# Performance work log

Hardware: AMD Instinct MI355X
Metric: run time of the kernel (lower is better)

The kernel has to match this reference:

```python
import jax, jax.numpy as jnp
import numpy as np
from jax import lax

EPS = 1e-07
B, H, W = 32, 120, 120
N_PRIM, PRIM_DIM = 16, 8          # 16 capsule types, 8-d pose
N_SEC, SEC_DIM = 10, 16           # 10 secondary capsules, 16-d
FLAT = 9216                       # 16 * 24 * 24
R_ITERS = 3
REC_DIM = H * W * 3               # 43200


def _conv(x, w, b, stride):
    # NHWC input, HWIO kernel, VALID padding
    y = lax.conv_general_dilated(x, w, (stride, stride), 'VALID',
                                 dimension_numbers=('NHWC', 'HWIO', 'NHWC'))
    return y + b


def _squash(s):
    s_norm = jnp.linalg.norm(s, axis=-1, keepdims=True)
    sq = jnp.square(s_norm)
    return sq / (1.0 + sq) * s / (s_norm + EPS)


def setup_inputs() -> dict:
    key = jax.random.key(0)
    ks = jax.random.split(key, 13)
    p = lambda k, shp, s=0.05: (jax.random.normal(k, shp, dtype=jnp.float32) * s)
    inp = {
        'input_x': jax.random.normal(ks[0], (B, H, W, 3), dtype=jnp.float32),
        'y':       jax.random.uniform(ks[1], (B, N_SEC), dtype=jnp.float32),
        'conv1_w': p(ks[2], (9, 9, 3, 256)),
        'conv1_b': jnp.zeros((256,), jnp.float32),
        'conv2_w': p(ks[3], (9, 9, 256, N_PRIM * PRIM_DIM)),
        'conv2_b': jnp.zeros((N_PRIM * PRIM_DIM,), jnp.float32),
        'w_pose':  p(ks[4], (1, FLAT, N_SEC, SEC_DIM, PRIM_DIM)),
        'w1': p(ks[5], (N_SEC * SEC_DIM, 512)), 'b1': jnp.zeros((512,), jnp.float32),
        'w2': p(ks[6], (512, 1024)),            'b2': jnp.zeros((1024,), jnp.float32),
        'w3': p(ks[7], (1024, REC_DIM)),        'b3': jnp.zeros((REC_DIM,), jnp.float32),
    }
    return inp


def reference(input_x, y, conv1_w, conv1_b, conv2_w, conv2_b, w_pose,
              w1, b1, w2, b2, w3, b3):
    b = input_x.shape[0]
    # feature extraction
    x = jax.nn.relu(_conv(input_x, conv1_w, conv1_b, 2))   # [B,56,56,256]
    x = _conv(x, conv2_w, conv2_b, 2)                      # [B,24,24,128]
    u = x.reshape(b, FLAT, PRIM_DIM)                       # [B,9216,8]
    # u_hat[b,n,c,d] = sum_p w_pose[0,n,c,d,p] * u[b,n,p]
    u_hat = jnp.einsum('ncdp,bnp->bncd', w_pose[0], u)     # [B,9216,10,16]
    # dynamic routing
    logits = jnp.zeros((b, FLAT, N_SEC, 1), jnp.float32)
    v = None
    for _ in range(R_ITERS):
        c = jax.nn.softmax(logits, axis=-2)                # over secondary caps
        s = jnp.sum(c * u_hat, axis=1, keepdims=True)      # [B,1,10,16]
        v = _squash(s)
        agreement = jnp.sum(u_hat * v, axis=-1, keepdims=True)  # [B,9216,10,1]
        logits = logits + agreement
    # masking + reconstruction
    mask = y[:, None, :, None]                             # [B,1,10,1]
    v_flat = (mask * v).reshape(b, -1)                     # [B,160]
    h = jax.nn.relu(v_flat @ w1 + b1)
    h = jax.nn.relu(h @ w2 + b2)
    rec = jax.nn.sigmoid(h @ w3 + b3)                      # [B,43200]
    return v, rec
```

## Files before the change

kernel.cpp:

```cpp
#include <hip/hip_runtime.h>
#include <hip/hip_bf16.h>

typedef unsigned short u16;
typedef unsigned int   u32;
typedef __attribute__((ext_vector_type(8))) __bf16 bf16x8;
typedef __attribute__((ext_vector_type(4))) float  f32x4;

#define EPSQ 1e-7f
#define KSPLIT 9
#define KPB 2304
#define KSTEPS 72
#define FC3SPL 8

#define GLDS16(gp, lp) __builtin_amdgcn_global_load_lds( \
    (const __attribute__((address_space(1))) void*)(gp), \
    (__attribute__((address_space(3))) void*)(lp), 16, 0, 0)

__device__ __forceinline__ u16 f2bf(float f){
  u32 u = __float_as_uint(f);
  u32 r = (u + 0x7fffu + ((u >> 16) & 1u)) >> 16;
  return (u16)r;
}
__device__ __forceinline__ float bf2f(u16 h){ return __uint_as_float(((u32)h) << 16); }
__device__ __forceinline__ float blo(u32 w){ return __uint_as_float(w << 16); }
__device__ __forceinline__ float bhi(u32 w){ return __uint_as_float(w & 0xffff0000u); }

__global__ __launch_bounds__(256) void k_im2col(const float* __restrict__ x, u16* __restrict__ A1){
  const int id = blockIdx.x*256 + threadIdx.x;
  const int m  = id >> 5;
  const int s  = id & 31;
  const int b  = m / 3136;
  const int r  = m - b*3136;
  const int oy = r / 56;
  const int ox = r - oy*56;
  const float* xb = x + ((size_t)b*120 + 2*oy)*120*3 + 2*ox*3;
  u16 vals[8];
  #pragma unroll
  for (int j=0;j<8;++j){
    int k = s*8 + j;
    if (k < 243){
      int ky = k / 27;
      int rem = k - ky*27;
      vals[j] = f2bf(xb[(size_t)ky*360 + rem]);
    } else vals[j] = 0;
  }
  *reinterpret_cast<uint4*>(A1 + (size_t)m*256 + s*8) = *reinterpret_cast<uint4*>(vals);
}

__global__ __launch_bounds__(256) void k_wt1(const float* __restrict__ w, u16* __restrict__ wt){
  __shared__ float tile[32][33];
  const int k0 = blockIdx.x*32;
  const int c0 = blockIdx.y*32;
  const int c  = threadIdx.x & 31;
  const int r8 = threadIdx.x >> 5;
  #pragma unroll
  for (int rr=0; rr<4; ++rr){
    int r = r8*4+rr;
    tile[r][c] = (k0+r < 243) ? w[(size_t)(k0+r)*256 + c0 + c] : 0.f;
  }
  __syncthreads();
  #pragma unroll
  for (int rr=0; rr<4; ++rr){
    int r = r8*4+rr;
    wt[(size_t)(c0+r)*256 + k0 + c] = f2bf(tile[c][r]);
  }
}

__global__ __launch_bounds__(256) void k_gemm1(const u16* __restrict__ A1,
    const u16* __restrict__ w1t, const float* __restrict__ bias, u16* __restrict__ a1b){
  __shared__ __align__(16) u16 As[2][4096];
  __shared__ __align__(16) u16 Bs[2][4096];
  const int t  = threadIdx.x;
  const int bx = blockIdx.x;
  const int by = blockIdx.y;
  const int row0 = t>>2, slot = t&3;
  const int wid = t>>6, lane = t&63;
  const int wr = wid>>1, wc = wid&1, lr = lane&15, lq = lane>>4;
  const size_t srcA0 = (size_t)(bx*128 + row0)*256 + slot*8;
  const size_t srcA1 = srcA0 + (size_t)64*256;
  const size_t srcB0 = (size_t)(by*128 + row0)*256 + slot*8;
  const size_t srcB1 = srcB0 + (size_t)64*256;
  f32x4 acc[4][4];
  #pragma unroll
  for (int i=0;i<4;++i)
    #pragma unroll
    for (int j=0;j<4;++j) acc[i][j] = (f32x4){0.f,0.f,0.f,0.f};

  auto stage = [&](int step, int buf){
    const int k0 = step*32;
    GLDS16(A1 + srcA0 + k0, &As[buf][wid*512]);
    GLDS16(A1 + srcA1 + k0, &As[buf][wid*512 + 2048]);
    GLDS16(w1t + srcB0 + k0, &Bs[buf][wid*512]);
    GLDS16(w1t + srcB1 + k0, &Bs[buf][wid*512 + 2048]);
  };
  auto compute = [&](int buf){
    bf16x8 af[4], bfv[4];
    #pragma unroll
    for (int mi=0;mi<4;++mi)
      af[mi] = *reinterpret_cast<const bf16x8*>(&As[buf][(wr*64 + mi*16 + lr)*32 + lq*8]);
    #pragma unroll
    for (int ni=0;ni<4;++ni)
      bfv[ni] = *reinterpret_cast<const bf16x8*>(&Bs[buf][(wc*64 + ni*16 + lr)*32 + lq*8]);
    #pragma unroll
    for (int mi=0;mi<4;++mi)
      #pragma unroll
      for (int ni=0;ni<4;++ni)
        acc[mi][ni] = __builtin_amdgcn_mfma_f32_16x16x32_bf16(af[mi], bfv[ni], acc[mi][ni], 0, 0, 0);
  };

  stage(0, 0);
  __syncthreads();
  for (int step=0; step<8; step+=2){
    stage(step+1, 1);
    compute(0);
    __syncthreads();
    if (step+2 < 8) stage(step+2, 0);
    compute(1);
    __syncthreads();
  }

  #pragma unroll
  for (int ni=0;ni<4;++ni){
    int colg = by*128 + wc*64 + ni*16 + lr;
    float bv = bias[colg];
    #pragma unroll
    for (int mi=0;mi<4;++mi){
      #pragma unroll
      for (int r=0;r<4;++r){
        int rowg = bx*128 + wr*64 + mi*16 + lq*4 + r;
        float v = fmaxf(acc[mi][ni][r] + bv, 0.f);
        a1b[(size_t)rowg*256 + colg] = f2bf(v);
      }
    }
  }
}

__global__ __launch_bounds__(256) void k_wt(const float* __restrict__ w, u16* __restrict__ wt){
  __shared__ float tile[32][33];
  const int k0 = blockIdx.x*32;
  const int c0 = blockIdx.y*32;
  const int c  = threadIdx.x & 31;
  const int r8 = threadIdx.x >> 5;
  #pragma unroll
  for (int rr=0; rr<4; ++rr){
    int r = r8*4+rr;
    tile[r][c] = w[(size_t)(k0+r)*128 + c0 + c];
  }
  __syncthreads();
  #pragma unroll
  for (int rr=0; rr<4; ++rr){
    int r = r8*4+rr;
    wt[(size_t)(c0+r)*20736 + k0 + c] = f2bf(tile[c][r]);
  }
}

__global__ __launch_bounds__(256) void k_conv2(const u16* __restrict__ a1b,
    const u16* __restrict__ w2t, float* __restrict__ part){
  __shared__ __align__(16) u16 As[2][4096];
  __shared__ __align__(16) u16 Bs[2][4096];
  const int t  = threadIdx.x;
  const int bx = blockIdx.x;
  const int ks = blockIdx.y;
  const int row0 = t>>2, slot = t&3;
  int gA[2]; int gB[2];
  #pragma unroll
  for (int q=0;q<2;++q){
    int m  = bx*128 + row0 + q*64;
    int bb = m/576; int r = m - bb*576; int oy = r/24; int ox = r - oy*24;
    gA[q] = ((bb*56 + 2*oy)*56 + 2*ox)*256 + slot*8;
    int col = row0 + q*64;
    gB[q] = col*20736 + slot*8;
  }
  const int wid = t>>6, lane = t&63;
  const int wr = wid>>1, wc = wid&1, lr = lane&15, lq = lane>>4;
  f32x4 acc[4][4];
  #pragma unroll
  for (int i=0;i<4;++i)
    #pragma unroll
    for (int j=0;j<4;++j) acc[i][j] = (f32x4){0.f,0.f,0.f,0.f};
  const int kbase = ks*KPB;

  auto stage = [&](int step, int buf){
    const int k0  = kbase + step*32;
    const int kk  = k0 >> 8;
    const int ky  = kk/9;
    const int kx  = kk - ky*9;
    const int ic0 = k0 & 255;
    const int soff = (ky*56 + kx)*256 + ic0;
    GLDS16(a1b + gA[0] + soff, &As[buf][wid*512]);
    GLDS16(a1b + gA[1] + soff, &As[buf][wid*512 + 2048]);
    GLDS16(w2t + gB[0] + k0,  &Bs[buf][wid*512]);
    GLDS16(w2t + gB[1] + k0,  &Bs[buf][wid*512 + 2048]);
  };
  auto compute = [&](int buf){
    bf16x8 af[4], bfv[4];
    #pragma unroll
    for (int mi=0;mi<4;++mi)
      af[mi] = *reinterpret_cast<const bf16x8*>(&As[buf][(wr*64 + mi*16 + lr)*32 + lq*8]);
    #pragma unroll
    for (int ni=0;ni<4;++ni)
      bfv[ni] = *reinterpret_cast<const bf16x8*>(&Bs[buf][(wc*64 + ni*16 + lr)*32 + lq*8]);
    #pragma unroll
    for (int mi=0;mi<4;++mi)
      #pragma unroll
      for (int ni=0;ni<4;++ni)
        acc[mi][ni] = __builtin_amdgcn_mfma_f32_16x16x32_bf16(af[mi], bfv[ni], acc[mi][ni], 0, 0, 0);
  };

  stage(0, 0);
  __syncthreads();
  for (int step=0; step<KSTEPS; step+=2){
    stage(step+1, 1);
    compute(0);
    __syncthreads();
    if (step+2 < KSTEPS) stage(step+2, 0);
    compute(1);
    __syncthreads();
  }

  const size_t base = ((size_t)ks*18432 + (size_t)bx*128)*128;
  #pragma unroll
  for (int mi=0;mi<4;++mi){
    #pragma unroll
    for (int ni=0;ni<4;++ni){
      int col = wc*64 + ni*16 + lr;
      #pragma unroll
      for (int r=0;r<4;++r){
        int row = wr*64 + mi*16 + lq*4 + r;
        part[base + (size_t)row*128 + col] = acc[mi][ni][r];
      }
    }
  }
}

__global__ __launch_bounds__(256) void k_comb(const float* __restrict__ part,
    const float* __restrict__ bias, float* __restrict__ u){
  const int i4 = blockIdx.x*256 + threadIdx.x;
  const float4* b4 = reinterpret_cast<const float4*>(bias);
  float4 s = b4[i4 & 31];
  const float4* p4 = reinterpret_cast<const float4*>(part);
  #pragma unroll
  for (int ks=0; ks<KSPLIT; ++ks){
    float4 p = p4[(size_t)ks*589824 + i4];
    s.x += p.x; s.y += p.y; s.z += p.z; s.w += p.w;
  }
  reinterpret_cast<float4*>(u)[i4] = s;
}

__global__ __launch_bounds__(256) void k_uhat(const float* __restrict__ u,
    const float* __restrict__ wpose, u16* __restrict__ uhat){
  __shared__ float Wn[1280];
  __shared__ float us[256];
  const int n = blockIdx.x;
  const int t = threadIdx.x;
  #pragma unroll
  for (int j=0;j<5;++j) Wn[t + j*256] = wpose[(size_t)n*1280 + t + j*256];
  us[t] = u[((size_t)(t>>3)*9216 + n)*8 + (t&7)];
  __syncthreads();
  const int b = t>>3, d0 = (t&7)*2;
  float uv[8];
  #pragma unroll
  for (int p=0;p<8;++p) uv[p] = us[b*8+p];
  for (int c=0;c<10;++c){
    const float* w0 = &Wn[(c*16 + d0)*8];
    float v0=0.f, v1=0.f;
    #pragma unroll
    for (int p=0;p<8;++p){ v0 = fmaf(w0[p], uv[p], v0); v1 = fmaf(w0[8+p], uv[p], v1); }
    u32 pk = (u32)f2bf(v0) | ((u32)f2bf(v1) << 16);
    *reinterpret_cast<u32*>(uhat + ((((size_t)b*10 + c)*9216 + n)*16 + d0)) = pk;
  }
}

template<int ITER>
__global__ __launch_bounds__(256) void k_route(const u16* __restrict__ uhat,
    const float* __restrict__ spin, float* __restrict__ logi,
    float* __restrict__ spout){
  const int ch = blockIdx.x;
  const int b  = blockIdx.y;
  const int t  = threadIdx.x;
  const int n  = ch*256 + t;
  __shared__ float vl[160];
  __shared__ float sq[160];
  __shared__ float wlds[10][257];
  __shared__ float pacc[10][16][33];
  if (ITER >= 2){
    float sv = 0.f;
    if (t < 160){
      #pragma unroll 4
      for (int c2=0;c2<36;++c2) sv += spin[((size_t)c2*32 + b)*160 + t];
      sq[t] = sv*sv;
    }
    __syncthreads();
    if (t < 160){
      int cc = t >> 4;
      float ss = 0.f;
      #pragma unroll
      for (int j=0;j<16;++j) ss += sq[cc*16 + j];
      float nrm = sqrtf(ss);
      vl[t] = (ss/(1.f+ss)) * sv / (nrm + EPSQ);
    }
    __syncthreads();
  }
  float w[10];
  if (ITER == 1){
    #pragma unroll
    for (int c=0;c<10;++c) w[c] = 0.1f;
  } else {
    float l[10];
    #pragma unroll
    for (int c=0;c<10;++c){
      const u16* up = uhat + ((((size_t)b*10 + c)*9216 + n) << 4);
      const uint4 q0 = *reinterpret_cast<const uint4*>(up);
      const uint4 q1 = *reinterpret_cast<const uint4*>(up + 8);
      const float* v = &vl[c*16];
      float dot = blo(q0.x)*v[0] + bhi(q0.x)*v[1]
                + blo(q0.y)*v[2] + bhi(q0.y)*v[3]
                + blo(q0.z)*v[4] + bhi(q0.z)*v[5]
                + blo(q0.w)*v[6] + bhi(q0.w)*v[7]
                + blo(q1.x)*v[8] + bhi(q1.x)*v[9]
                + blo(q1.y)*v[10]+ bhi(q1.y)*v[11]
                + blo(q1.z)*v[12]+ bhi(q1.z)*v[13]
                + blo(q1.w)*v[14]+ bhi(q1.w)*v[15];
      size_t li = ((size_t)b*10 + c)*9216 + n;
      float lc = dot;
      if (ITER == 3) lc += logi[li];
      if (ITER == 2) logi[li] = lc;
      l[c] = lc;
    }
    float mx = l[0];
    #pragma unroll
    for (int c=1;c<10;++c) mx = fmaxf(mx, l[c]);
    float s = 0.f;
    #pragma unroll
    for (int c=0;c<10;++c){ w[c] = __expf(l[c]-mx); s += w[c]; }
    float inv = 1.f/s;
    #pragma unroll
    for (int c=0;c<10;++c) w[c] *= inv;
  }
  #pragma unroll
  for (int c=0;c<10;++c) wlds[c][t] = w[c];
  __syncthreads();

  const int nl = t>>3, dp = t&7;
  float a0[10], a1[10];
  #pragma unroll
  for (int c=0;c<10;++c){ a0[c]=0.f; a1[c]=0.f; }
  #pragma unroll
  for (int c=0;c<10;++c){
    const u32* ub = reinterpret_cast<const u32*>(
        uhat + ((((size_t)b*10 + c)*9216 + (size_t)ch*256) << 4));
    float acc0 = 0.f, acc1 = 0.f;
    #pragma unroll
    for (int chunk=0; chunk<8; ++chunk){
      u32 v = ub[chunk*256 + t];
      float wv = wlds[c][chunk*32 + nl];
      acc0 = fmaf(wv, blo(v), acc0);
      acc1 = fmaf(wv, bhi(v), acc1);
    }
    a0[c] = acc0; a1[c] = acc1;
  }
  #pragma unroll
  for (int c=0;c<10;++c){
    pacc[c][2*dp  ][nl] = a0[c];
    pacc[c][2*dp+1][nl] = a1[c];
  }
  __syncthreads();
  if (t < 160){
    const int c = t >> 4, d = t & 15;
    float acc = 0.f;
    #pragma unroll
    for (int j=0;j<32;++j) acc += pacc[c][d][j];
    spout[((size_t)ch*32 + b)*160 + t] = acc;
  }
}

__global__ __launch_bounds__(1024) void k_head(const float* __restrict__ y,
    const float* __restrict__ spin, const float* __restrict__ w1,
    const float* __restrict__ b1, const float* __restrict__ w2,
    const float* __restrict__ b2, float* __restrict__ dout_v,
    float* __restrict__ h2T){
  const int b = blockIdx.x;
  const int t = threadIdx.x;
  __shared__ float vl[160];
  __shared__ float sq[160];
  __shared__ float h1s[512];
  float sv = 0.f;
  if (t < 160){
    #pragma unroll 4
    for (int c2=0;c2<36;++c2) sv += spin[((size_t)c2*32 + b)*160 + t];
    sq[t] = sv*sv;
  }
  __syncthreads();
  if (t < 160){
    int cc = t >> 4;
    float ss = 0.f;
    #pragma unroll
    for (int j=0;j<16;++j) ss += sq[cc*16 + j];
    float nrm = sqrtf(ss);
    float vv = (ss/(1.f+ss)) * sv / (nrm + EPSQ);
    dout_v[(size_t)b*160 + t] = vv;
    vl[t] = vv * y[b*10 + cc];
  }
  __syncthreads();
  if (t < 512){
    float acc = b1[t];
    for (int k=0;k<160;++k) acc = fmaf(vl[k], w1[(size_t)k*512 + t], acc);
    h1s[t] = fmaxf(acc, 0.f);
  }
  __syncthreads();
  float acc = b2[t];
  for (int k=0;k<512;++k) acc = fmaf(h1s[k], w2[(size_t)k*1024 + t], acc);
  h2T[(size_t)t*32 + b] = fmaxf(acc, 0.f);
}

__global__ __launch_bounds__(256) void k_fc3p(const float* __restrict__ h2T,
    const float* __restrict__ w3, float* __restrict__ fp){
  __shared__ float4 hs4[128][8];
  const int t  = threadIdx.x;
  const int oc = blockIdx.x*256 + t;
  const int ks = blockIdx.y;
  const float4* src = reinterpret_cast<const float4*>(h2T + (size_t)ks*128*32);
  #pragma unroll
  for (int r=0;r<4;++r)
    (&hs4[0][0])[t + r*256] = src[t + r*256];
  __syncthreads();
  const bool ok = oc < 43200;
  float a[32];
  #pragma unroll
  for (int b=0;b<32;++b) a[b] = 0.f;
  const size_t wbase = (size_t)ks*128*43200 + (size_t)(ok ? oc : 0);
  #pragma unroll 4
  for (int k=0;k<128;++k){
    float wv = w3[wbase + (size_t)k*43200];
    #pragma unroll
    for (int q=0;q<8;++q){
      float4 hv = hs4[k][q];
      a[q*4+0] = fmaf(hv.x, wv, a[q*4+0]);
      a[q*4+1] = fmaf(hv.y, wv, a[q*4+1]);
      a[q*4+2] = fmaf(hv.z, wv, a[q*4+2]);
      a[q*4+3] = fmaf(hv.w, wv, a[q*4+3]);
    }
  }
  if (ok){
    #pragma unroll
    for (int b=0;b<32;++b) fp[(size_t)(ks*32 + b)*43200 + oc] = a[b];
  }
}

__global__ __launch_bounds__(256) void k_fc3f(const float* __restrict__ fp,
    const float* __restrict__ b3, float* __restrict__ outr){
  const int i4 = blockIdx.x*256 + threadIdx.x;
  if (i4 >= 345600) return;
  const int b = i4 / 10800, oc4 = i4 - b*10800;
  const float4* b34 = reinterpret_cast<const float4*>(b3);
  float4 s = b34[oc4];
  const float4* fp4 = reinterpret_cast<const float4*>(fp);
  #pragma unroll
  for (int ks=0;ks<FC3SPL;++ks){
    float4 p = fp4[(size_t)(ks*32 + b)*10800 + oc4];
    s.x += p.x; s.y += p.y; s.z += p.z; s.w += p.w;
  }
  float4 o;
  o.x = 1.f/(1.f + __expf(-s.x));
  o.y = 1.f/(1.f + __expf(-s.y));
  o.z = 1.f/(1.f + __expf(-s.z));
  o.w = 1.f/(1.f + __expf(-s.w));
  reinterpret_cast<float4*>(outr)[i4] = o;
}

extern "C" void kernel_launch(void* const* d_in, const int* in_sizes, int n_in,
                              void* d_out, int out_size, void* d_ws, size_t ws_size,
                              hipStream_t stream){
  (void)in_sizes; (void)n_in; (void)out_size; (void)ws_size;
  const float* x     = (const float*)d_in[0];
  const float* y     = (const float*)d_in[1];
  const float* c1w   = (const float*)d_in[2];
  const float* c1b   = (const float*)d_in[3];
  const float* c2w   = (const float*)d_in[4];
  const float* c2b   = (const float*)d_in[5];
  const float* wpose = (const float*)d_in[6];
  const float* w1    = (const float*)d_in[7];
  const float* b1    = (const float*)d_in[8];
  const float* w2    = (const float*)d_in[9];
  const float* b2    = (const float*)d_in[10];
  const float* w3    = (const float*)d_in[11];
  const float* b3    = (const float*)d_in[12];
  float* out = (float*)d_out;

  char* ws = (char*)d_ws;
  u16*   a1bp  = (u16*)(ws + 0);
  u16*   A1col = (u16*)(ws + 52000000);
  float* partp = (float*)(ws + 52000000);
  u16*   uhatp = (u16*)(ws + 0);
  u16*   w1tp  = (u16*)(ws + 138000000);
  u16*   w2tp  = (u16*)(ws + 138500000);
  float* up    = (float*)(ws + 144000000);
  float* logip = (float*)(ws + 154000000);
  float* spA   = (float*)(ws + 166000000);
  float* spB   = (float*)(ws + 166800000);
  float* h2Tp  = (float*)(ws + 167600000);
  float* fc3pp = (float*)(ws + 0);

  k_im2col<<<dim3(12544),  256, 0, stream>>>(x, A1col);
  k_wt1   <<<dim3(8,8),    256, 0, stream>>>(c1w, w1tp);
  k_wt    <<<dim3(648,4),  256, 0, stream>>>(c2w, w2tp);
  k_gemm1 <<<dim3(784,2),  256, 0, stream>>>(A1col, w1tp, c1b, a1bp);
  k_conv2 <<<dim3(144,KSPLIT), 256, 0, stream>>>(a1bp, w2tp, partp);
  k_comb  <<<dim3(2304),   256, 0, stream>>>(partp, c2b, up);
  k_uhat  <<<dim3(9216),   256, 0, stream>>>(up, wpose, uhatp);

  k_route<1><<<dim3(36,32), 256, 0, stream>>>(uhatp, spB, logip, spA);
  k_route<2><<<dim3(36,32), 256, 0, stream>>>(uhatp, spA, logip, spB);
  k_route<3><<<dim3(36,32), 256, 0, stream>>>(uhatp, spB, logip, spA);

  k_head <<<dim3(32),   1024, 0, stream>>>(y, spA, w1, b1, w2, b2, out, h2Tp);
  k_fc3p <<<dim3(169,FC3SPL), 256, 0, stream>>>(h2Tp, w3, fc3pp);
  k_fc3f <<<dim3(1350), 256, 0, stream>>>(fc3pp, b3, out + 5120);
}
```

Baseline: 538.6 us.

## Use vmcnt-based double buffering in GEMMs and split head kernel across blocks

The conv1 and conv2 GEMM main loops now issue the next stage's global-to-LDS loads and then wait with s_waitcnt vmcnt(4) plus raw s_barrier, replacing full __syncthreads drains. The intent is to keep prefetches in flight while the current tile is computed. Separately, the head kernel moves from 32 blocks of 1024 threads to 32x4 blocks of 256 threads, so the FC2 output columns are spread over more workgroups. Each block recomputes FC1 redundantly, and the vmcnt(4) value depends on each thread issuing exactly four loads per stage.

```diff
diff --git a/kernel.cpp b/kernel.cpp
--- a/kernel.cpp
+++ b/kernel.cpp
@@ -109,14 +109,20 @@
   };
 
   stage(0, 0);
-  __syncthreads();
-  for (int step=0; step<8; step+=2){
-    stage(step+1, 1);
-    compute(0);
-    __syncthreads();
-    if (step+2 < 8) stage(step+2, 0);
-    compute(1);
-    __syncthreads();
+  int cur = 0;
+  for (int step=0; step<8; ++step){
+    if (step+1 < 8){
+      stage(step+1, cur^1);
+      asm volatile("s_waitcnt vmcnt(4)" ::: "memory");
+    } else {
+      asm volatile("s_waitcnt vmcnt(0)" ::: "memory");
+    }
+    __builtin_amdgcn_s_barrier();
+    __builtin_amdgcn_sched_barrier(0);
+    compute(cur);
+    __builtin_amdgcn_s_barrier();
+    __builtin_amdgcn_sched_barrier(0);
+    cur ^= 1;
   }
 
   #pragma unroll
@@ -208,14 +214,20 @@
   };
 
   stage(0, 0);
-  __syncthreads();
-  for (int step=0; step<KSTEPS; step+=2){
-    stage(step+1, 1);
-    compute(0);
-    __syncthreads();
-    if (step+2 < KSTEPS) stage(step+2, 0);
-    compute(1);
-    __syncthreads();
+  int cur = 0;
+  for (int step=0; step<KSTEPS; ++step){
+    if (step+1 < KSTEPS){
+      stage(step+1, cur^1);
+      asm volatile("s_waitcnt vmcnt(4)" ::: "memory");
+    } else {
+      asm volatile("s_waitcnt vmcnt(0)" ::: "memory");
+    }
+    __builtin_amdgcn_s_barrier();
+    __builtin_amdgcn_sched_barrier(0);
+    compute(cur);
+    __builtin_amdgcn_s_barrier();
+    __builtin_amdgcn_sched_barrier(0);
+    cur ^= 1;
   }
 
   const size_t base = ((size_t)ks*18432 + (size_t)bx*128)*128;
@@ -374,12 +386,13 @@
   }
 }
 
-__global__ __launch_bounds__(1024) void k_head(const float* __restrict__ y,
+__global__ __launch_bounds__(256) void k_head(const float* __restrict__ y,
     const float* __restrict__ spin, const float* __restrict__ w1,
     const float* __restrict__ b1, const float* __restrict__ w2,
     const float* __restrict__ b2, float* __restrict__ dout_v,
     float* __restrict__ h2T){
   const int b = blockIdx.x;
+  const int q = blockIdx.y;
   const int t = threadIdx.x;
   __shared__ float vl[160];
   __shared__ float sq[160];
@@ -398,19 +411,22 @@
     for (int j=0;j<16;++j) ss += sq[cc*16 + j];
     float nrm = sqrtf(ss);
     float vv = (ss/(1.f+ss)) * sv / (nrm + EPSQ);
-    dout_v[(size_t)b*160 + t] = vv;
+    if (q == 0) dout_v[(size_t)b*160 + t] = vv;
     vl[t] = vv * y[b*10 + cc];
   }
   __syncthreads();
-  if (t < 512){
-    float acc = b1[t];
-    for (int k=0;k<160;++k) acc = fmaf(vl[k], w1[(size_t)k*512 + t], acc);
-    h1s[t] = fmaxf(acc, 0.f);
-  }
-  __syncthreads();
-  float acc = b2[t];
-  for (int k=0;k<512;++k) acc = fmaf(h1s[k], w2[(size_t)k*1024 + t], acc);
-  h2T[(size_t)t*32 + b] = fmaxf(acc, 0.f);
+  #pragma unroll
+  for (int j=0;j<2;++j){
+    const int oc = j*256 + t;
+    float acc = b1[oc];
+    for (int k=0;k<160;++k) acc = fmaf(vl[k], w1[(size_t)k*512 + oc], acc);
+    h1s[oc] = fmaxf(acc, 0.f);
+  }
+  __syncthreads();
+  const int oc2 = q*256 + t;
+  float acc = b2[oc2];
+  for (int k=0;k<512;++k) acc = fmaf(h1s[k], w2[(size_t)k*1024 + oc2], acc);
+  h2T[(size_t)oc2*32 + b] = fmaxf(acc, 0.f);
 }
 
 __global__ __launch_bounds__(256) void k_fc3p(const float* __restrict__ h2T,
@@ -513,7 +529,7 @@
   k_route<2><<<dim3(36,32), 256, 0, stream>>>(uhatp, spA, logip, spB);
   k_route<3><<<dim3(36,32), 256, 0, stream>>>(uhatp, spB, logip, spA);
 
-  k_head <<<dim3(32),   1024, 0, stream>>>(y, spA, w1, b1, w2, b2, out, h2Tp);
+  k_head <<<dim3(32,4), 256, 0, stream>>>(y, spA, w1, b1, w2, b2, out, h2Tp);
   k_fc3p <<<dim3(169,FC3SPL), 256, 0, stream>>>(h2Tp, w3, fc3pp);
   k_fc3f <<<dim3(1350), 256, 0, stream>>>(fc3pp, b3, out + 5120);
 }
```

Result: no change. 536.2 us (-0.5%).
